# Kernel optimization log

Measured on AMD Instinct MI355X. Metric: run time of the kernel, lower is better.

The kernel has to match this reference:

```python
import jax, jax.numpy as jnp
import numpy as np

HID = 256

def setup_inputs() -> dict:
    key = jax.random.key(0)
    ks = jax.random.split(key, 16)
    B, N, DIN, DOUT = 256, 1024, 64, 128
    def lin(k, fin, fout):
        kw, kb = jax.random.split(k)
        s = 1.0 / np.sqrt(fin)
        W = jax.random.uniform(kw, (fin, fout), jnp.float32, -s, s)
        b = jax.random.uniform(kb, (fout,), jnp.float32, -s, s)
        return W, b
    x = jax.random.normal(ks[0], (B, N, DIN), jnp.float32)
    mask = jax.random.randint(ks[1], (B, N), 0, 2) > 0
    pw1, pb1 = lin(ks[2], DIN, HID)
    pw2, pb2 = lin(ks[3], HID, HID)
    pw3, pb3 = lin(ks[4], HID, HID)
    rw1, rb1 = lin(ks[5], HID, HID)
    rw2, rb2 = lin(ks[6], HID, HID)
    rw3, rb3 = lin(ks[7], HID, DOUT)
    return dict(x=x, mask=mask, pw1=pw1, pb1=pb1, pw2=pw2, pb2=pb2, pw3=pw3, pb3=pb3,
                rw1=rw1, rb1=rb1, rw2=rw2, rb2=rb2, rw3=rw3, rb3=rb3)

def reference(x, mask, pw1, pb1, pw2, pb2, pw3, pb3, rw1, rb1, rw2, rb2, rw3, rb3):
    # x: [B, N, din], mask: [B, N] bool
    # phi per element (padding elements are zeroed before the pool, matching
    # the torch pack/pad pipeline which only runs phi on valid elements)
    h = jax.nn.relu(jnp.einsum('bnd,dh->bnh', x, pw1) + pb1)
    h = jax.nn.relu(jnp.einsum('bnh,hk->bnk', h, pw2) + pb2)
    h = jnp.einsum('bnh,hk->bnk', h, pw3) + pb3
    m = mask.astype(x.dtype)[..., None]                  # [B, N, 1]
    pooled = jnp.sum(h * m, axis=1)                      # [B, 256]
    o = jax.nn.relu(pooled @ rw1 + rb1)
    o = jax.nn.relu(o @ rw2 + rb2)
    o = o @ rw3 + rb3                                    # [B, dout]
    # rows with zero valid elements get exactly 0 (torch leaves res at 0.0)
    valid = jnp.any(mask, axis=1, keepdims=True)
    return jnp.where(valid, o, jnp.zeros((), dtype=o.dtype))
```

## Files before the change

### kernel.cpp

```cpp
#include <hip/hip_runtime.h>

namespace {
constexpr int NB = 256, NN = 1024, DIN = 64, HID = 256, DOUT = 128;
constexpr int SPLIT = 2, CHUNK = NN / SPLIT;
constexpr int MT = 64;

typedef __attribute__((ext_vector_type(8))) short bf16x8;
typedef __attribute__((ext_vector_type(4))) float f32x4;

constexpr size_t POOLED_OFF = 0;
constexpr size_t CNTS_OFF   = (size_t)NB * HID * 4;
constexpr size_t PW1_OFF    = CNTS_OFF + (size_t)NB * 4;
constexpr size_t PW2_OFF    = PW1_OFF + (size_t)DIN * HID * 2;
constexpr int ZERO_N = NB * HID + NB;

__device__ inline unsigned short f2bf(float f) {
    union { float f; unsigned u; } v; v.f = f;
    unsigned r = v.u + 0x7FFF + ((v.u >> 16) & 1);
    return (unsigned short)(r >> 16);
}
__device__ inline unsigned pk2(float lo, float hi) {
    return (unsigned)f2bf(lo) | ((unsigned)f2bf(hi) << 16);
}

__global__ void prep(const float* __restrict__ pw1, const float* __restrict__ pw2,
                     float* __restrict__ zero_base,
                     unsigned short* __restrict__ w1p, unsigned short* __restrict__ w2p) {
    int i = blockIdx.x * 256 + threadIdx.x;
    if (i < ZERO_N) zero_base[i] = 0.f;
    if (i < DIN * HID / 8) {
        int lane = i & 63, kk = (i >> 6) & 1, strip = i >> 7;
        int kbase = kk * 32 + ((lane >> 4) * 8);
        int n = strip * 16 + (lane & 15);
        const float* src = pw1 + (size_t)kbase * HID + n;
        float v[8];
#pragma unroll
        for (int j = 0; j < 8; ++j) v[j] = src[(size_t)j * HID];
        unsigned o[4] = {pk2(v[0],v[1]), pk2(v[2],v[3]), pk2(v[4],v[5]), pk2(v[6],v[7])};
        *(uint4*)(w1p + (size_t)i * 8) = *(const uint4*)o;
    }
    if (i < HID * HID / 8) {
        int lane = i & 63, kk = (i >> 6) & 7, strip = i >> 9;
        int kbase = kk * 32 + ((lane >> 4) * 8);
        int n = strip * 16 + (lane & 15);
        const float* src = pw2 + (size_t)kbase * HID + n;
        float v[8];
#pragma unroll
        for (int j = 0; j < 8; ++j) v[j] = src[(size_t)j * HID];
        unsigned o[4] = {pk2(v[0],v[1]), pk2(v[2],v[3]), pk2(v[4],v[5]), pk2(v[6],v[7])};
        *(uint4*)(w2p + (size_t)i * 8) = *(const uint4*)o;
    }
}

__launch_bounds__(512, 2)
__global__ void phi_pool(const float* __restrict__ x, const int* __restrict__ mask,
                         const float* __restrict__ pb1, const float* __restrict__ pb2,
                         const unsigned short* __restrict__ w1p,
                         const unsigned short* __restrict__ w2p,
                         float* __restrict__ pooled, int* __restrict__ cnts) {
    __shared__ unsigned short xs[2][MT * 64];
    __shared__ unsigned short h1s[MT * 256];
    __shared__ short vlist[CHUNK];
    __shared__ int cnt_s;

    const int b = blockIdx.x, sp = blockIdx.y, t = threadIdx.x;
    const int lane = t & 63, wq = t >> 6;
    const int quad = lane >> 4, l15 = lane & 15;

    if (t == 0) cnt_s = 0;
    __syncthreads();
    {
        int n = sp * CHUNK + t;
        if (mask[b * NN + n] != 0) { int i = atomicAdd(&cnt_s, 1); vlist[i] = (short)n; }
    }
    __syncthreads();
    const int cnt = cnt_s;
    if (t == 0) atomicAdd(&cnts[b], cnt);

    const uint4* w1q = (const uint4*)w1p;
    const uint4* w2q = (const uint4*)w2p;
    uint4 w2f[8][2];
#pragma unroll
    for (int j = 0; j < 2; ++j) {
        int strip = wq * 2 + j;
#pragma unroll
        for (int kk = 0; kk < 8; ++kk) w2f[kk][j] = w2q[(strip * 8 + kk) * 64 + lane];
    }
    float bias1[2], bias2[2];
#pragma unroll
    for (int j = 0; j < 2; ++j) {
        int c = wq * 32 + j * 16 + l15;
        bias1[j] = pb1[c]; bias2[j] = pb2[c];
    }

    float pool[2] = {0.f, 0.f};
    const float* xb = x + (size_t)b * NN * DIN;
    const int gr = t >> 3, seg8 = t & 7;
    const int xoff = gr * 64 + ((seg8 ^ (gr & 7)) << 3);

    {
        float4 a0 = make_float4(0.f,0.f,0.f,0.f), a1 = a0;
        if (gr < min(MT, cnt)) {
            const float4* p = (const float4*)(xb + (size_t)vlist[gr] * DIN + seg8 * 8);
            a0 = p[0]; a1 = p[1];
        }
        unsigned o[4] = {pk2(a0.x,a0.y), pk2(a0.z,a0.w), pk2(a1.x,a1.y), pk2(a1.z,a1.w)};
        *(uint4*)&xs[0][xoff] = *(const uint4*)o;
    }

    int cur = 0;
    for (int base = 0; base < cnt; base += MT) {
        uint4 w1t[2][2];
#pragma unroll
        for (int j = 0; j < 2; ++j)
#pragma unroll
            for (int kk = 0; kk < 2; ++kk)
                w1t[kk][j] = w1q[((wq * 2 + j) * 2 + kk) * 64 + lane];

        __syncthreads();

        f32x4 acc[4][2];
#pragma unroll
        for (int f = 0; f < 4; ++f)
#pragma unroll
            for (int j = 0; j < 2; ++j) acc[f][j] = (f32x4){0.f,0.f,0.f,0.f};
#pragma unroll
        for (int kk = 0; kk < 2; ++kk) {
            bf16x8 a[4];
#pragma unroll
            for (int f = 0; f < 4; ++f)
                a[f] = *(const bf16x8*)&xs[cur][(f*16 + l15)*64 + (((kk*4 + quad) ^ (l15 & 7)) << 3)];
#pragma unroll
            for (int j = 0; j < 2; ++j) {
                bf16x8 bw = __builtin_bit_cast(bf16x8, w1t[kk][j]);
#pragma unroll
                for (int f = 0; f < 4; ++f)
                    acc[f][j] = __builtin_amdgcn_mfma_f32_16x16x32_bf16(a[f], bw, acc[f][j], 0, 0, 0);
            }
        }
#pragma unroll
        for (int f = 0; f < 4; ++f)
#pragma unroll
            for (int j = 0; j < 2; ++j) {
                int col = wq * 32 + j * 16 + l15, kb = col >> 3, cl = col & 7;
#pragma unroll
                for (int r = 0; r < 4; ++r) {
                    int row = f * 16 + quad * 4 + r;
                    float h = fmaxf(acc[f][j][r] + bias1[j], 0.f);
                    h1s[row * 256 + ((kb ^ (row & 7)) << 3) + cl] = f2bf(h);
                }
            }

        float4 n0 = make_float4(0.f,0.f,0.f,0.f), n1 = n0;
        const bool hn = (base + MT) < cnt;
        if (hn && gr < cnt - (base + MT)) {
            const float4* p = (const float4*)(xb + (size_t)vlist[base + MT + gr] * DIN + seg8 * 8);
            n0 = p[0]; n1 = p[1];
        }
        __syncthreads();

        f32x4 acc2[4][2];
#pragma unroll
        for (int f = 0; f < 4; ++f)
#pragma unroll
            for (int j = 0; j < 2; ++j) acc2[f][j] = (f32x4){0.f,0.f,0.f,0.f};
#pragma unroll
        for (int kk = 0; kk < 8; ++kk) {
            bf16x8 a[4];
#pragma unroll
            for (int f = 0; f < 4; ++f)
                a[f] = *(const bf16x8*)&h1s[(f*16 + l15)*256 + (((kk*4 + quad) ^ (l15 & 7)) << 3)];
#pragma unroll
            for (int j = 0; j < 2; ++j) {
                bf16x8 bw = __builtin_bit_cast(bf16x8, w2f[kk][j]);
#pragma unroll
                for (int f = 0; f < 4; ++f)
                    acc2[f][j] = __builtin_amdgcn_mfma_f32_16x16x32_bf16(a[f], bw, acc2[f][j], 0, 0, 0);
            }
        }
        if (cnt - base >= MT) {
#pragma unroll
            for (int f = 0; f < 4; ++f)
#pragma unroll
                for (int r = 0; r < 4; ++r)
#pragma unroll
                    for (int j = 0; j < 2; ++j)
                        pool[j] += fmaxf(acc2[f][j][r] + bias2[j], 0.f);
        } else {
#pragma unroll
            for (int f = 0; f < 4; ++f)
#pragma unroll
                for (int r = 0; r < 4; ++r) {
                    bool v = (base + f * 16 + quad * 4 + r) < cnt;
#pragma unroll
                    for (int j = 0; j < 2; ++j) {
                        float h = fmaxf(acc2[f][j][r] + bias2[j], 0.f);
                        pool[j] += v ? h : 0.f;
                    }
                }
        }

        if (hn) {
            unsigned o[4] = {pk2(n0.x,n0.y), pk2(n0.z,n0.w), pk2(n1.x,n1.y), pk2(n1.z,n1.w)};
            *(uint4*)&xs[cur ^ 1][xoff] = *(const uint4*)o;
        }
        cur ^= 1;
    }

#pragma unroll
    for (int j = 0; j < 2; ++j) {
        float v = pool[j];
        v += __shfl_xor(v, 16, 64);
        v += __shfl_xor(v, 32, 64);
        if (quad == 0) atomicAdd(&pooled[b * HID + wq * 32 + j * 16 + l15], v);
    }
}

__device__ inline float4 dotseg(const float* __restrict__ buf, const float* __restrict__ W,
                                int c, int s) {
    const float4* W4 = (const float4*)W;
    float4 acc = make_float4(0.f, 0.f, 0.f, 0.f);
#pragma unroll 8
    for (int i = 0; i < 32; ++i) {
        int k = s * 32 + i;
        float bk = buf[k];
        float4 w = W4[(size_t)k * 64 + c];
        acc.x = fmaf(bk, w.x, acc.x);
        acc.y = fmaf(bk, w.y, acc.y);
        acc.z = fmaf(bk, w.z, acc.z);
        acc.w = fmaf(bk, w.w, acc.w);
    }
    return acc;
}

__launch_bounds__(512, 2)
__global__ void rho(const float* __restrict__ pooled, const int* __restrict__ cnts,
                    const float* __restrict__ pw3, const float* __restrict__ pb3,
                    const float* __restrict__ rw1, const float* __restrict__ rb1,
                    const float* __restrict__ rw2, const float* __restrict__ rb2,
                    const float* __restrict__ rw3, const float* __restrict__ rb3,
                    float* __restrict__ out) {
    __shared__ float bufA[HID], bufB[HID];
    __shared__ float part[8][HID];
    const int b = blockIdx.x, t = threadIdx.x;
    const int c = t & 63, s = t >> 6;
    const int cnt = cnts[b];
    if (t < HID) bufA[t] = pooled[b * HID + t];
    __syncthreads();

    {
        float4 p = dotseg(bufA, pw3, c, s);
        ((float4*)part[s])[c] = p;
        __syncthreads();
        if (t < HID) {
            float v = (float)cnt * pb3[t];
#pragma unroll
            for (int g = 0; g < 8; ++g) v += part[g][t];
            bufB[t] = v;
        }
        __syncthreads();
    }
    {
        float4 p = dotseg(bufB, rw1, c, s);
        ((float4*)part[s])[c] = p;
        __syncthreads();
        if (t < HID) {
            float v = rb1[t];
#pragma unroll
            for (int g = 0; g < 8; ++g) v += part[g][t];
            bufA[t] = fmaxf(v, 0.f);
        }
        __syncthreads();
    }
    {
        float4 p = dotseg(bufA, rw2, c, s);
        ((float4*)part[s])[c] = p;
        __syncthreads();
        if (t < HID) {
            float v = rb2[t];
#pragma unroll
            for (int g = 0; g < 8; ++g) v += part[g][t];
            bufB[t] = fmaxf(v, 0.f);
        }
        __syncthreads();
    }
    {
        const int c4 = t & 31, s4 = t >> 5;
        const float4* W4 = (const float4*)rw3;
        float4 acc = make_float4(0.f, 0.f, 0.f, 0.f);
#pragma unroll 8
        for (int i = 0; i < 16; ++i) {
            int k = s4 * 16 + i;
            float bk = bufB[k];
            float4 w = W4[(size_t)k * 32 + c4];
            acc.x = fmaf(bk, w.x, acc.x);
            acc.y = fmaf(bk, w.y, acc.y);
            acc.z = fmaf(bk, w.z, acc.z);
            acc.w = fmaf(bk, w.w, acc.w);
        }
        float* part2 = &part[0][0];
        ((float4*)(part2 + s4 * DOUT))[c4] = acc;
        __syncthreads();
        if (t < DOUT) {
            float v = rb3[t];
#pragma unroll
            for (int g = 0; g < 16; ++g) v += part2[g * DOUT + t];
            out[b * DOUT + t] = (cnt > 0) ? v : 0.f;
        }
    }
}
}

extern "C" void kernel_launch(void* const* d_in, const int* in_sizes, int n_in,
                              void* d_out, int out_size, void* d_ws, size_t ws_size,
                              hipStream_t stream) {
    const float* x    = (const float*)d_in[0];
    const int*   mask = (const int*)  d_in[1];
    const float* pw1  = (const float*)d_in[2];
    const float* pb1  = (const float*)d_in[3];
    const float* pw2  = (const float*)d_in[4];
    const float* pb2  = (const float*)d_in[5];
    const float* pw3  = (const float*)d_in[6];
    const float* pb3  = (const float*)d_in[7];
    const float* rw1  = (const float*)d_in[8];
    const float* rb1  = (const float*)d_in[9];
    const float* rw2  = (const float*)d_in[10];
    const float* rb2  = (const float*)d_in[11];
    const float* rw3  = (const float*)d_in[12];
    const float* rb3  = (const float*)d_in[13];
    float* out = (float*)d_out;

    float* pooled       = (float*)((char*)d_ws + POOLED_OFF);
    int*   cnts         = (int*)  ((char*)d_ws + CNTS_OFF);
    unsigned short* w1p = (unsigned short*)((char*)d_ws + PW1_OFF);
    unsigned short* w2p = (unsigned short*)((char*)d_ws + PW2_OFF);

    prep<<<dim3(257), dim3(256), 0, stream>>>(pw1, pw2, (float*)d_ws, w1p, w2p);
    phi_pool<<<dim3(NB, SPLIT), dim3(512), 0, stream>>>(x, mask, pb1, pb2, w1p, w2p, pooled, cnts);
    rho<<<dim3(NB), dim3(512), 0, stream>>>(pooled, cnts, pw3, pb3,
                                            rw1, rb1, rw2, rb2, rw3, rb3, out);
}
```

Before: 152.7 us.

## Drop prep kernel; convert weights in-block and write per-split partials

```diff
diff --git a/kernel.cpp b/kernel.cpp
--- a/kernel.cpp
+++ b/kernel.cpp
@@ -1,4 +1,5 @@
 #include <hip/hip_runtime.h>
+#include <hip/hip_bf16.h>
 
 namespace {
 constexpr int NB = 256, NN = 1024, DIN = 64, HID = 256, DOUT = 128;
@@ -9,55 +10,22 @@
 typedef __attribute__((ext_vector_type(4))) float f32x4;
 
 constexpr size_t POOLED_OFF = 0;
-constexpr size_t CNTS_OFF   = (size_t)NB * HID * 4;
-constexpr size_t PW1_OFF    = CNTS_OFF + (size_t)NB * 4;
-constexpr size_t PW2_OFF    = PW1_OFF + (size_t)DIN * HID * 2;
-constexpr int ZERO_N = NB * HID + NB;
-
-__device__ inline unsigned short f2bf(float f) {
-    union { float f; unsigned u; } v; v.f = f;
-    unsigned r = v.u + 0x7FFF + ((v.u >> 16) & 1);
-    return (unsigned short)(r >> 16);
-}
+constexpr size_t CNTS_OFF   = (size_t)NB * SPLIT * HID * 4;
+
 __device__ inline unsigned pk2(float lo, float hi) {
-    return (unsigned)f2bf(lo) | ((unsigned)f2bf(hi) << 16);
-}
-
-__global__ void prep(const float* __restrict__ pw1, const float* __restrict__ pw2,
-                     float* __restrict__ zero_base,
-                     unsigned short* __restrict__ w1p, unsigned short* __restrict__ w2p) {
-    int i = blockIdx.x * 256 + threadIdx.x;
-    if (i < ZERO_N) zero_base[i] = 0.f;
-    if (i < DIN * HID / 8) {
-        int lane = i & 63, kk = (i >> 6) & 1, strip = i >> 7;
-        int kbase = kk * 32 + ((lane >> 4) * 8);
-        int n = strip * 16 + (lane & 15);
-        const float* src = pw1 + (size_t)kbase * HID + n;
-        float v[8];
-#pragma unroll
-        for (int j = 0; j < 8; ++j) v[j] = src[(size_t)j * HID];
-        unsigned o[4] = {pk2(v[0],v[1]), pk2(v[2],v[3]), pk2(v[4],v[5]), pk2(v[6],v[7])};
-        *(uint4*)(w1p + (size_t)i * 8) = *(const uint4*)o;
-    }
-    if (i < HID * HID / 8) {
-        int lane = i & 63, kk = (i >> 6) & 7, strip = i >> 9;
-        int kbase = kk * 32 + ((lane >> 4) * 8);
-        int n = strip * 16 + (lane & 15);
-        const float* src = pw2 + (size_t)kbase * HID + n;
-        float v[8];
-#pragma unroll
-        for (int j = 0; j < 8; ++j) v[j] = src[(size_t)j * HID];
-        unsigned o[4] = {pk2(v[0],v[1]), pk2(v[2],v[3]), pk2(v[4],v[5]), pk2(v[6],v[7])};
-        *(uint4*)(w2p + (size_t)i * 8) = *(const uint4*)o;
-    }
+    __hip_bfloat162 h = __float22bfloat162_rn(make_float2(lo, hi));
+    unsigned u; __builtin_memcpy(&u, &h, 4); return u;
+}
+__device__ inline unsigned short bf1(float f) {
+    __hip_bfloat16 h = __float2bfloat16(f);
+    unsigned short u; __builtin_memcpy(&u, &h, 2); return u;
 }
 
 __launch_bounds__(512, 2)
 __global__ void phi_pool(const float* __restrict__ x, const int* __restrict__ mask,
-                         const float* __restrict__ pb1, const float* __restrict__ pb2,
-                         const unsigned short* __restrict__ w1p,
-                         const unsigned short* __restrict__ w2p,
-                         float* __restrict__ pooled, int* __restrict__ cnts) {
+                         const float* __restrict__ pw1, const float* __restrict__ pb1,
+                         const float* __restrict__ pw2, const float* __restrict__ pb2,
+                         float* __restrict__ pooled2, int* __restrict__ cnts2) {
     __shared__ unsigned short xs[2][MT * 64];
     __shared__ unsigned short h1s[MT * 256];
     __shared__ short vlist[CHUNK];
@@ -73,18 +41,29 @@
         int n = sp * CHUNK + t;
         if (mask[b * NN + n] != 0) { int i = atomicAdd(&cnt_s, 1); vlist[i] = (short)n; }
     }
-    __syncthreads();
-    const int cnt = cnt_s;
-    if (t == 0) atomicAdd(&cnts[b], cnt);
-
-    const uint4* w1q = (const uint4*)w1p;
-    const uint4* w2q = (const uint4*)w2p;
-    uint4 w2f[8][2];
-#pragma unroll
-    for (int j = 0; j < 2; ++j) {
-        int strip = wq * 2 + j;
-#pragma unroll
-        for (int kk = 0; kk < 8; ++kk) w2f[kk][j] = w2q[(strip * 8 + kk) * 64 + lane];
+
+    uint4 w1f[2][2], w2f[8][2];
+#pragma unroll
+    for (int jj = 0; jj < 2; ++jj) {
+        int n = (wq * 2 + jj) * 16 + l15;
+#pragma unroll
+        for (int kk = 0; kk < 2; ++kk) {
+            const float* src = pw1 + (size_t)(kk * 32 + quad * 8) * HID + n;
+            float v[8];
+#pragma unroll
+            for (int j = 0; j < 8; ++j) v[j] = src[(size_t)j * HID];
+            unsigned o[4] = {pk2(v[0],v[1]), pk2(v[2],v[3]), pk2(v[4],v[5]), pk2(v[6],v[7])};
+            __builtin_memcpy(&w1f[kk][jj], o, 16);
+        }
+#pragma unroll
+        for (int kk = 0; kk < 8; ++kk) {
+            const float* src = pw2 + (size_t)(kk * 32 + quad * 8) * HID + n;
+            float v[8];
+#pragma unroll
+            for (int j = 0; j < 8; ++j) v[j] = src[(size_t)j * HID];
+            unsigned o[4] = {pk2(v[0],v[1]), pk2(v[2],v[3]), pk2(v[4],v[5]), pk2(v[6],v[7])};
+            __builtin_memcpy(&w2f[kk][jj], o, 16);
+        }
     }
     float bias1[2], bias2[2];
 #pragma unroll
@@ -92,6 +71,10 @@
         int c = wq * 32 + j * 16 + l15;
         bias1[j] = pb1[c]; bias2[j] = pb2[c];
     }
+
+    __syncthreads();
+    const int cnt = cnt_s;
+    if (t == 0) cnts2[b * SPLIT + sp] = cnt;
 
     float pool[2] = {0.f, 0.f};
     const float* xb = x + (size_t)b * NN * DIN;
@@ -110,13 +93,6 @@
 
     int cur = 0;
     for (int base = 0; base < cnt; base += MT) {
-        uint4 w1t[2][2];
-#pragma unroll
-        for (int j = 0; j < 2; ++j)
-#pragma unroll
-            for (int kk = 0; kk < 2; ++kk)
-                w1t[kk][j] = w1q[((wq * 2 + j) * 2 + kk) * 64 + lane];
-
         __syncthreads();
 
         f32x4 acc[4][2];
@@ -132,7 +108,7 @@
                 a[f] = *(const bf16x8*)&xs[cur][(f*16 + l15)*64 + (((kk*4 + quad) ^ (l15 & 7)) << 3)];
 #pragma unroll
             for (int j = 0; j < 2; ++j) {
-                bf16x8 bw = __builtin_bit_cast(bf16x8, w1t[kk][j]);
+                bf16x8 bw = __builtin_bit_cast(bf16x8, w1f[kk][j]);
 #pragma unroll
                 for (int f = 0; f < 4; ++f)
                     acc[f][j] = __builtin_amdgcn_mfma_f32_16x16x32_bf16(a[f], bw, acc[f][j], 0, 0, 0);
@@ -147,7 +123,7 @@
                 for (int r = 0; r < 4; ++r) {
                     int row = f * 16 + quad * 4 + r;
                     float h = fmaxf(acc[f][j][r] + bias1[j], 0.f);
-                    h1s[row * 256 + ((kb ^ (row & 7)) << 3) + cl] = f2bf(h);
+                    h1s[row * 256 + ((kb ^ (row & 7)) << 3) + cl] = bf1(h);
                 }
             }
 
@@ -212,7 +188,7 @@
         float v = pool[j];
         v += __shfl_xor(v, 16, 64);
         v += __shfl_xor(v, 32, 64);
-        if (quad == 0) atomicAdd(&pooled[b * HID + wq * 32 + j * 16 + l15], v);
+        if (quad == 0) pooled2[(size_t)(b * SPLIT + sp) * HID + wq * 32 + j * 16 + l15] = v;
     }
 }
 
@@ -234,7 +210,7 @@
 }
 
 __launch_bounds__(512, 2)
-__global__ void rho(const float* __restrict__ pooled, const int* __restrict__ cnts,
+__global__ void rho(const float* __restrict__ pooled2, const int* __restrict__ cnts2,
                     const float* __restrict__ pw3, const float* __restrict__ pb3,
                     const float* __restrict__ rw1, const float* __restrict__ rb1,
                     const float* __restrict__ rw2, const float* __restrict__ rb2,
@@ -244,8 +220,10 @@
     __shared__ float part[8][HID];
     const int b = blockIdx.x, t = threadIdx.x;
     const int c = t & 63, s = t >> 6;
-    const int cnt = cnts[b];
-    if (t < HID) bufA[t] = pooled[b * HID + t];
+    const int cnt = cnts2[b * SPLIT] + cnts2[b * SPLIT + 1];
+    if (t < HID)
+        bufA[t] = pooled2[(size_t)(b * SPLIT) * HID + t]
+                + pooled2[(size_t)(b * SPLIT + 1) * HID + t];
     __syncthreads();
 
     {
@@ -330,13 +308,11 @@
     const float* rb3  = (const float*)d_in[13];
     float* out = (float*)d_out;
 
-    float* pooled       = (float*)((char*)d_ws + POOLED_OFF);
-    int*   cnts         = (int*)  ((char*)d_ws + CNTS_OFF);
-    unsigned short* w1p = (unsigned short*)((char*)d_ws + PW1_OFF);
-    unsigned short* w2p = (unsigned short*)((char*)d_ws + PW2_OFF);
-
-    prep<<<dim3(257), dim3(256), 0, stream>>>(pw1, pw2, (float*)d_ws, w1p, w2p);
-    phi_pool<<<dim3(NB, SPLIT), dim3(512), 0, stream>>>(x, mask, pb1, pb2, w1p, w2p, pooled, cnts);
-    rho<<<dim3(NB), dim3(512), 0, stream>>>(pooled, cnts, pw3, pb3,
+    float* pooled2 = (float*)((char*)d_ws + POOLED_OFF);
+    int*   cnts2   = (int*)  ((char*)d_ws + CNTS_OFF);
+
+    phi_pool<<<dim3(NB, SPLIT), dim3(512), 0, stream>>>(x, mask, pw1, pb1, pw2, pb2,
+                                                        pooled2, cnts2);
+    rho<<<dim3(NB), dim3(512), 0, stream>>>(pooled2, cnts2, pw3, pb3,
                                             rw1, rb1, rw2, rb2, rw3, rb3, out);
 }
```

Result: slower. 160.1 us (+4.9%).

## Replace pooled atomics with per-split partials and hoist W1 fragment loads

Applied to the files above, without the earlier changes.

```diff
diff --git a/kernel.cpp b/kernel.cpp
--- a/kernel.cpp
+++ b/kernel.cpp
@@ -9,10 +9,9 @@
 typedef __attribute__((ext_vector_type(4))) float f32x4;
 
 constexpr size_t POOLED_OFF = 0;
-constexpr size_t CNTS_OFF   = (size_t)NB * HID * 4;
-constexpr size_t PW1_OFF    = CNTS_OFF + (size_t)NB * 4;
+constexpr size_t CNTS_OFF   = (size_t)NB * SPLIT * HID * 4;
+constexpr size_t PW1_OFF    = CNTS_OFF + (size_t)NB * SPLIT * 4;
 constexpr size_t PW2_OFF    = PW1_OFF + (size_t)DIN * HID * 2;
-constexpr int ZERO_N = NB * HID + NB;
 
 __device__ inline unsigned short f2bf(float f) {
     union { float f; unsigned u; } v; v.f = f;
@@ -22,12 +21,13 @@
 __device__ inline unsigned pk2(float lo, float hi) {
     return (unsigned)f2bf(lo) | ((unsigned)f2bf(hi) << 16);
 }
+__device__ inline void lds_barrier() {
+    asm volatile("s_waitcnt lgkmcnt(0)\n\ts_barrier" ::: "memory");
+}
 
 __global__ void prep(const float* __restrict__ pw1, const float* __restrict__ pw2,
-                     float* __restrict__ zero_base,
                      unsigned short* __restrict__ w1p, unsigned short* __restrict__ w2p) {
     int i = blockIdx.x * 256 + threadIdx.x;
-    if (i < ZERO_N) zero_base[i] = 0.f;
     if (i < DIN * HID / 8) {
         int lane = i & 63, kk = (i >> 6) & 1, strip = i >> 7;
         int kbase = kk * 32 + ((lane >> 4) * 8);
@@ -57,7 +57,7 @@
                          const float* __restrict__ pb1, const float* __restrict__ pb2,
                          const unsigned short* __restrict__ w1p,
                          const unsigned short* __restrict__ w2p,
-                         float* __restrict__ pooled, int* __restrict__ cnts) {
+                         float* __restrict__ pooled2, int* __restrict__ cnts2) {
     __shared__ unsigned short xs[2][MT * 64];
     __shared__ unsigned short h1s[MT * 256];
     __shared__ short vlist[CHUNK];
@@ -73,16 +73,15 @@
         int n = sp * CHUNK + t;
         if (mask[b * NN + n] != 0) { int i = atomicAdd(&cnt_s, 1); vlist[i] = (short)n; }
     }
-    __syncthreads();
-    const int cnt = cnt_s;
-    if (t == 0) atomicAdd(&cnts[b], cnt);
 
     const uint4* w1q = (const uint4*)w1p;
     const uint4* w2q = (const uint4*)w2p;
-    uint4 w2f[8][2];
+    uint4 w1f[2][2], w2f[8][2];
 #pragma unroll
     for (int j = 0; j < 2; ++j) {
         int strip = wq * 2 + j;
+#pragma unroll
+        for (int kk = 0; kk < 2; ++kk) w1f[kk][j] = w1q[(strip * 2 + kk) * 64 + lane];
 #pragma unroll
         for (int kk = 0; kk < 8; ++kk) w2f[kk][j] = w2q[(strip * 8 + kk) * 64 + lane];
     }
@@ -92,6 +91,10 @@
         int c = wq * 32 + j * 16 + l15;
         bias1[j] = pb1[c]; bias2[j] = pb2[c];
     }
+
+    __syncthreads();
+    const int cnt = cnt_s;
+    if (t == 0) cnts2[b * SPLIT + sp] = cnt;
 
     float pool[2] = {0.f, 0.f};
     const float* xb = x + (size_t)b * NN * DIN;
@@ -110,14 +113,14 @@
 
     int cur = 0;
     for (int base = 0; base < cnt; base += MT) {
-        uint4 w1t[2][2];
-#pragma unroll
-        for (int j = 0; j < 2; ++j)
-#pragma unroll
-            for (int kk = 0; kk < 2; ++kk)
-                w1t[kk][j] = w1q[((wq * 2 + j) * 2 + kk) * 64 + lane];
-
-        __syncthreads();
+        lds_barrier();
+
+        float4 n0 = make_float4(0.f,0.f,0.f,0.f), n1 = n0;
+        const bool hn = (base + MT) < cnt;
+        if (hn && gr < cnt - (base + MT)) {
+            const float4* p = (const float4*)(xb + (size_t)vlist[base + MT + gr] * DIN + seg8 * 8);
+            n0 = p[0]; n1 = p[1];
+        }
 
         f32x4 acc[4][2];
 #pragma unroll
@@ -132,7 +135,7 @@
                 a[f] = *(const bf16x8*)&xs[cur][(f*16 + l15)*64 + (((kk*4 + quad) ^ (l15 & 7)) << 3)];
 #pragma unroll
             for (int j = 0; j < 2; ++j) {
-                bf16x8 bw = __builtin_bit_cast(bf16x8, w1t[kk][j]);
+                bf16x8 bw = __builtin_bit_cast(bf16x8, w1f[kk][j]);
 #pragma unroll
                 for (int f = 0; f < 4; ++f)
                     acc[f][j] = __builtin_amdgcn_mfma_f32_16x16x32_bf16(a[f], bw, acc[f][j], 0, 0, 0);
@@ -151,13 +154,7 @@
                 }
             }
 
-        float4 n0 = make_float4(0.f,0.f,0.f,0.f), n1 = n0;
-        const bool hn = (base + MT) < cnt;
-        if (hn && gr < cnt - (base + MT)) {
-            const float4* p = (const float4*)(xb + (size_t)vlist[base + MT + gr] * DIN + seg8 * 8);
-            n0 = p[0]; n1 = p[1];
-        }
-        __syncthreads();
+        lds_barrier();
 
         f32x4 acc2[4][2];
 #pragma unroll
@@ -212,7 +209,7 @@
         float v = pool[j];
         v += __shfl_xor(v, 16, 64);
         v += __shfl_xor(v, 32, 64);
-        if (quad == 0) atomicAdd(&pooled[b * HID + wq * 32 + j * 16 + l15], v);
+        if (quad == 0) pooled2[(size_t)(b * SPLIT + sp) * HID + wq * 32 + j * 16 + l15] = v;
     }
 }
 
@@ -234,7 +231,7 @@
 }
 
 __launch_bounds__(512, 2)
-__global__ void rho(const float* __restrict__ pooled, const int* __restrict__ cnts,
+__global__ void rho(const float* __restrict__ pooled2, const int* __restrict__ cnts2,
                     const float* __restrict__ pw3, const float* __restrict__ pb3,
                     const float* __restrict__ rw1, const float* __restrict__ rb1,
                     const float* __restrict__ rw2, const float* __restrict__ rb2,
@@ -244,8 +241,10 @@
     __shared__ float part[8][HID];
     const int b = blockIdx.x, t = threadIdx.x;
     const int c = t & 63, s = t >> 6;
-    const int cnt = cnts[b];
-    if (t < HID) bufA[t] = pooled[b * HID + t];
+    const int cnt = cnts2[b * SPLIT] + cnts2[b * SPLIT + 1];
+    if (t < HID)
+        bufA[t] = pooled2[(size_t)(b * SPLIT) * HID + t]
+                + pooled2[(size_t)(b * SPLIT + 1) * HID + t];
     __syncthreads();
 
     {
@@ -330,13 +329,14 @@
     const float* rb3  = (const float*)d_in[13];
     float* out = (float*)d_out;
 
-    float* pooled       = (float*)((char*)d_ws + POOLED_OFF);
-    int*   cnts         = (int*)  ((char*)d_ws + CNTS_OFF);
+    float* pooled2      = (float*)((char*)d_ws + POOLED_OFF);
+    int*   cnts2        = (int*)  ((char*)d_ws + CNTS_OFF);
     unsigned short* w1p = (unsigned short*)((char*)d_ws + PW1_OFF);
     unsigned short* w2p = (unsigned short*)((char*)d_ws + PW2_OFF);
 
-    prep<<<dim3(257), dim3(256), 0, stream>>>(pw1, pw2, (float*)d_ws, w1p, w2p);
-    phi_pool<<<dim3(NB, SPLIT), dim3(512), 0, stream>>>(x, mask, pb1, pb2, w1p, w2p, pooled, cnts);
-    rho<<<dim3(NB), dim3(512), 0, stream>>>(pooled, cnts, pw3, pb3,
+    prep<<<dim3(32), dim3(256), 0, stream>>>(pw1, pw2, w1p, w2p);
+    phi_pool<<<dim3(NB, SPLIT), dim3(512), 0, stream>>>(x, mask, pb1, pb2, w1p, w2p,
+                                                        pooled2, cnts2);
+    rho<<<dim3(NB), dim3(512), 0, stream>>>(pooled2, cnts2, pw3, pb3,
                                             rw1, rb1, rw2, rb2, rw3, rb3, out);
 }
```

Result: no change. 154.1 us (+0.9%).
